# Performance work log

Hardware: AMD Instinct MI355X
Metric: run time of the kernel (lower is better)

Reference implementation:

```python
import jax, jax.numpy as jnp
import numpy as np

N_NODES = 100000
N_EDGES = 3200000
IN_DIM = 128


def setup_inputs() -> dict:
    key = jax.random.key(0)
    ks = jax.random.split(key, 6)
    x = jax.random.normal(ks[0], (N_NODES, IN_DIM), dtype=jnp.float32)
    edge_index = jax.random.randint(ks[1], (2, N_EDGES), 0, N_NODES, dtype=jnp.int64)
    # Glorot-ish init for weights, zero bias (PyG GCNConv default has bias)
    W1 = jax.random.normal(ks[2], (IN_DIM, 32), dtype=jnp.float32) / np.sqrt(IN_DIM)
    b1 = jnp.zeros((32,), dtype=jnp.float32)
    W2 = jax.random.normal(ks[3], (32, 16), dtype=jnp.float32) / np.sqrt(32.0)
    b2 = jnp.zeros((16,), dtype=jnp.float32)
    Wf = jax.random.normal(ks[4], (16, 1), dtype=jnp.float32) / np.sqrt(16.0)
    bf = jnp.zeros((1,), dtype=jnp.float32)
    return {"x": x, "edge_index": edge_index, "W1": W1, "b1": b1,
            "W2": W2, "b2": b2, "Wf": Wf, "bf": bf}


def reference(x, edge_index, W1, b1, W2, b2, Wf, bf):
    N = x.shape[0]
    # PyG GCNConv: add self-loops, symmetric normalization D^-1/2 (A+I) D^-1/2
    loop = jnp.arange(N, dtype=edge_index.dtype)
    src = jnp.concatenate([edge_index[0], loop])  # message sources (x_j)
    dst = jnp.concatenate([edge_index[1], loop])  # aggregation targets
    deg = jax.ops.segment_sum(jnp.ones_like(dst, dtype=x.dtype), dst, num_segments=N)
    dinv = jax.lax.rsqrt(jnp.maximum(deg, 1.0))  # deg >= 1 due to self-loops
    norm = dinv[src] * dinv[dst]                  # per-edge coefficient

    def gcn_conv(h, W, b):
        h = h @ W                                 # linear transform first (small dim)
        msg = h[src] * norm[:, None]              # gather + scale
        return jax.ops.segment_sum(msg, dst, num_segments=N) + b  # scatter-add

    h = jax.nn.relu(gcn_conv(x, W1, b1))
    h = jax.nn.relu(gcn_conv(h, W2, b2))
    return (h @ Wf + bf).squeeze(-1)              # [N]
```

## Files before the change

kernel.cpp:

```cpp
#include <hip/hip_runtime.h>


#define TPB 256
#define NBUCK 512
#define BCAP 8192
#define CHUNK 4096

__device__ __forceinline__ unsigned f2bf(float f) {
    unsigned u = __float_as_uint(f);
    return (u + 0x7FFFu + ((u >> 16) & 1u)) >> 16;
}
__device__ __forceinline__ float bflo(unsigned u) { return __uint_as_float(u << 16); }
__device__ __forceinline__ float bfhi(unsigned u) { return __uint_as_float(u & 0xFFFF0000u); }

__device__ __forceinline__ int excl_scan_512(int v, int* wsum, int tid) {
    int lane = tid & 63, wv = tid >> 6;
    int x = v;
#pragma unroll
    for (int d = 1; d < 64; d <<= 1) {
        int y = __shfl_up(x, d, 64);
        if (lane >= d) x += y;
    }
    if (lane == 63) wsum[wv] = x;
    __syncthreads();
    if (tid < 64) {
        int s = (lane < 8) ? wsum[lane] : 0;
#pragma unroll
        for (int d = 1; d < 8; d <<= 1) {
            int y = __shfl_up(s, d, 64);
            if (lane >= d) s += y;
        }
        if (lane < 8) wsum[lane] = s;
    }
    __syncthreads();
    int base = (wv > 0) ? wsum[wv - 1] : 0;
    return base + x - v;
}

__global__ __launch_bounds__(512) void binA2_kernel(
        const int* __restrict__ src, const int* __restrict__ dst,
        int* __restrict__ bcur, unsigned* __restrict__ staging, int E, int NPB) {
    __shared__ unsigned packed[CHUNK];
    __shared__ unsigned short buckb[CHUNK];
    __shared__ int hist[NBUCK];
    __shared__ int lstart[NBUCK];
    __shared__ int lcur[NBUCK];
    __shared__ int gbase[NBUCK];
    __shared__ int wsum[8];
    int tid = threadIdx.x;
    int start = blockIdx.x * CHUNK;
    int sz = min(CHUNK, E - start);

    unsigned dreg[8], sreg[8];
    hist[tid] = 0;
#pragma unroll
    for (int c = 0; c < 8; ++c) {
        int i = tid + c * 512;
        if (i < sz) {
            dreg[c] = (unsigned)dst[start + i];
            sreg[c] = (unsigned)src[start + i];
        } else {
            dreg[c] = 0xFFFFFFFFu;
        }
    }
    __syncthreads();
#pragma unroll
    for (int c = 0; c < 8; ++c)
        if (dreg[c] != 0xFFFFFFFFu) atomicAdd(&hist[dreg[c] / (unsigned)NPB], 1);
    __syncthreads();
    int v = hist[tid];
    int excl = excl_scan_512(v, wsum, tid);
    lstart[tid] = excl;
    lcur[tid] = 0;
    gbase[tid] = atomicAdd(&bcur[tid], v);
    __syncthreads();
#pragma unroll
    for (int c = 0; c < 8; ++c) {
        if (dreg[c] == 0xFFFFFFFFu) continue;
        unsigned d = dreg[c];
        unsigned b = d / (unsigned)NPB;
        unsigned loc = d - b * (unsigned)NPB;
        int pos = atomicAdd(&lcur[b], 1);
        int si = lstart[b] + pos;
        packed[si] = (loc << 20) | sreg[c];
        buckb[si] = (unsigned short)b;
    }
    __syncthreads();
    for (int i = tid; i < sz; i += 512) {
        unsigned b = buckb[i];
        int dsti = gbase[b] + (i - lstart[b]);
        if (dsti < BCAP)
            staging[(size_t)b * BCAP + dsti] = packed[i];
    }
}

__global__ __launch_bounds__(512) void bbase_kernel(
        const int* __restrict__ bcur, int* __restrict__ bbase) {
    __shared__ int wsum[8];
    int tid = threadIdx.x;
    int v = min(bcur[tid], BCAP);
    bbase[tid] = excl_scan_512(v, wsum, tid);
}

__global__ __launch_bounds__(512) void buildB_kernel(
        const int* __restrict__ bcur, const int* __restrict__ bbase,
        const unsigned* __restrict__ staging,
        int* __restrict__ offs, int* __restrict__ counts,
        float* __restrict__ dinv, int* __restrict__ csr_src,
        int N, int NPB) {
    __shared__ int hist[512];
    __shared__ int cur[512];
    __shared__ int wsum[8];
    int b = blockIdx.x;
    int tid = threadIdx.x;
    int sz = min(bcur[b], BCAP);
    int base = bbase[b];
    int n0 = b * NPB;
    int nn = min(NPB, N - n0);
    const unsigned* se = staging + (size_t)b * BCAP;

    unsigned preg[16];
    hist[tid] = 0;
#pragma unroll
    for (int c = 0; c < 16; ++c) {
        int i = tid + c * 512;
        preg[c] = (i < sz) ? se[i] : 0xFFFFFFFFu;
    }
    __syncthreads();
#pragma unroll
    for (int c = 0; c < 16; ++c)
        if (preg[c] != 0xFFFFFFFFu) atomicAdd(&hist[preg[c] >> 20], 1);
    __syncthreads();
    int h = hist[tid];
    int excl = excl_scan_512(h, wsum, tid);
    cur[tid] = excl;
    if (tid < nn) {
        int node = n0 + tid;
        offs[node] = base + excl;
        counts[node] = h;
        dinv[node] = rsqrtf((float)(h + 1));
    }
    __syncthreads();
#pragma unroll
    for (int c = 0; c < 16; ++c) {
        unsigned p = preg[c];
        if (p == 0xFFFFFFFFu) continue;
        int pos = atomicAdd(&cur[p >> 20], 1);
        csr_src[base + pos] = (int)(p & 0xFFFFFu);
    }
}

__global__ __launch_bounds__(256) void gemm1_kernel(
        const float* __restrict__ x, const float* __restrict__ W1,
        const float* __restrict__ dinv, unsigned* __restrict__ xwd, int N) {
    __shared__ float ws_[128 * 32];
    for (int i = threadIdx.x; i < 128 * 32; i += 256) ws_[i] = W1[i];
    __syncthreads();
    int t = threadIdx.x;
    int jq = (t & 3) * 8;
    int n0 = blockIdx.x * 128 + (t >> 2) * 2;
    if (n0 >= N) return;
    int nc0 = min(n0 + 0, N - 1);
    int nc1 = min(n0 + 1, N - 1);
    const float4* xr0 = (const float4*)(x + (size_t)nc0 * 128);
    const float4* xr1 = (const float4*)(x + (size_t)nc1 * 128);
    float acc[2][8];
#pragma unroll
    for (int n = 0; n < 2; ++n)
#pragma unroll
        for (int j = 0; j < 8; ++j) acc[n][j] = 0.0f;
#pragma unroll 2
    for (int k4 = 0; k4 < 32; ++k4) {
        const float* wb = ws_ + (k4 * 4) * 32 + jq;
        float4 a0 = *(const float4*)(wb);
        float4 a1 = *(const float4*)(wb + 4);
        float4 b0 = *(const float4*)(wb + 32);
        float4 b1v = *(const float4*)(wb + 36);
        float4 c0 = *(const float4*)(wb + 64);
        float4 c1 = *(const float4*)(wb + 68);
        float4 d0 = *(const float4*)(wb + 96);
        float4 d1 = *(const float4*)(wb + 100);
        float4 xv0 = xr0[k4];
        float4 xv1 = xr1[k4];
#pragma unroll
        for (int n = 0; n < 2; ++n) {
            float4 xv = (n == 0) ? xv0 : xv1;
            acc[n][0] += xv.x * a0.x + xv.y * b0.x + xv.z * c0.x + xv.w * d0.x;
            acc[n][1] += xv.x * a0.y + xv.y * b0.y + xv.z * c0.y + xv.w * d0.y;
            acc[n][2] += xv.x * a0.z + xv.y * b0.z + xv.z * c0.z + xv.w * d0.z;
            acc[n][3] += xv.x * a0.w + xv.y * b0.w + xv.z * c0.w + xv.w * d0.w;
            acc[n][4] += xv.x * a1.x + xv.y * b1v.x + xv.z * c1.x + xv.w * d1.x;
            acc[n][5] += xv.x * a1.y + xv.y * b1v.y + xv.z * c1.y + xv.w * d1.y;
            acc[n][6] += xv.x * a1.z + xv.y * b1v.z + xv.z * c1.z + xv.w * d1.z;
            acc[n][7] += xv.x * a1.w + xv.y * b1v.w + xv.z * c1.w + xv.w * d1.w;
        }
    }
#pragma unroll
    for (int n = 0; n < 2; ++n) {
        int node = n0 + n;
        if (node >= N) break;
        float d = dinv[node];
        unsigned pk0 = f2bf(acc[n][0] * d) | (f2bf(acc[n][1] * d) << 16);
        unsigned pk1 = f2bf(acc[n][2] * d) | (f2bf(acc[n][3] * d) << 16);
        unsigned pk2 = f2bf(acc[n][4] * d) | (f2bf(acc[n][5] * d) << 16);
        unsigned pk3 = f2bf(acc[n][6] * d) | (f2bf(acc[n][7] * d) << 16);
        ((uint4*)(xwd + (size_t)node * 16))[t & 3] = make_uint4(pk0, pk1, pk2, pk3);
    }
}

__global__ __launch_bounds__(256) void aggF_kernel(
        const int* __restrict__ offs, const int* __restrict__ counts,
        const int* __restrict__ csr_src, const float* __restrict__ dinv,
        const unsigned* __restrict__ xwd, const float* __restrict__ b1,
        const float* __restrict__ W2, unsigned* __restrict__ h2wd, int N) {
    __shared__ float ws2[32 * 16];
    for (int i = threadIdx.x; i < 512; i += 256) ws2[i] = W2[i];
    __syncthreads();
    int t = threadIdx.x;
    int q = t & 3;
    int node = blockIdx.x * 64 + (t >> 2);
    if (node >= N) return;
    int off = offs[node];
    int deg = counts[node];
    float acc[8];
    {
        uint4 v = ((const uint4*)(xwd + (size_t)node * 16))[q];
        acc[0] = bflo(v.x); acc[1] = bfhi(v.x);
        acc[2] = bflo(v.y); acc[3] = bfhi(v.y);
        acc[4] = bflo(v.z); acc[5] = bfhi(v.z);
        acc[6] = bflo(v.w); acc[7] = bfhi(v.w);
    }
    int deg8 = deg & ~7;
    int idx[8];
    if (deg8 > 0) {
#pragma unroll
        for (int c = 0; c < 8; ++c) idx[c] = csr_src[off + c];
    }
    int i = 0;
    while (i < deg8) {
        uint4 v0 = ((const uint4*)(xwd + (size_t)idx[0] * 16))[q];
        uint4 v1 = ((const uint4*)(xwd + (size_t)idx[1] * 16))[q];
        uint4 v2 = ((const uint4*)(xwd + (size_t)idx[2] * 16))[q];
        uint4 v3 = ((const uint4*)(xwd + (size_t)idx[3] * 16))[q];
        uint4 v4 = ((const uint4*)(xwd + (size_t)idx[4] * 16))[q];
        uint4 v5 = ((const uint4*)(xwd + (size_t)idx[5] * 16))[q];
        uint4 v6 = ((const uint4*)(xwd + (size_t)idx[6] * 16))[q];
        uint4 v7 = ((const uint4*)(xwd + (size_t)idx[7] * 16))[q];
        i += 8;
        if (i < deg8) {
#pragma unroll
            for (int c = 0; c < 8; ++c) idx[c] = csr_src[off + i + c];
        }
        acc[0] += ((bflo(v0.x) + bflo(v1.x)) + (bflo(v2.x) + bflo(v3.x)))
                + ((bflo(v4.x) + bflo(v5.x)) + (bflo(v6.x) + bflo(v7.x)));
        acc[1] += ((bfhi(v0.x) + bfhi(v1.x)) + (bfhi(v2.x) + bfhi(v3.x)))
                + ((bfhi(v4.x) + bfhi(v5.x)) + (bfhi(v6.x) + bfhi(v7.x)));
        acc[2] += ((bflo(v0.y) + bflo(v1.y)) + (bflo(v2.y) + bflo(v3.y)))
                + ((bflo(v4.y) + bflo(v5.y)) + (bflo(v6.y) + bflo(v7.y)));
        acc[3] += ((bfhi(v0.y) + bfhi(v1.y)) + (bfhi(v2.y) + bfhi(v3.y)))
                + ((bfhi(v4.y) + bfhi(v5.y)) + (bfhi(v6.y) + bfhi(v7.y)));
        acc[4] += ((bflo(v0.z) + bflo(v1.z)) + (bflo(v2.z) + bflo(v3.z)))
                + ((bflo(v4.z) + bflo(v5.z)) + (bflo(v6.z) + bflo(v7.z)));
        acc[5] += ((bfhi(v0.z) + bfhi(v1.z)) + (bfhi(v2.z) + bfhi(v3.z)))
                + ((bfhi(v4.z) + bfhi(v5.z)) + (bfhi(v6.z) + bfhi(v7.z)));
        acc[6] += ((bflo(v0.w) + bflo(v1.w)) + (bflo(v2.w) + bflo(v3.w)))
                + ((bflo(v4.w) + bflo(v5.w)) + (bflo(v6.w) + bflo(v7.w)));
        acc[7] += ((bfhi(v0.w) + bfhi(v1.w)) + (bfhi(v2.w) + bfhi(v3.w)))
                + ((bfhi(v4.w) + bfhi(v5.w)) + (bfhi(v6.w) + bfhi(v7.w)));
    }
    for (; i < deg; ++i) {
        int s = csr_src[off + i];
        uint4 v = ((const uint4*)(xwd + (size_t)s * 16))[q];
        acc[0] += bflo(v.x); acc[1] += bfhi(v.x);
        acc[2] += bflo(v.y); acc[3] += bfhi(v.y);
        acc[4] += bflo(v.z); acc[5] += bfhi(v.z);
        acc[6] += bflo(v.w); acc[7] += bfhi(v.w);
    }
    float dv = dinv[node];
    float part[16];
#pragma unroll
    for (int j = 0; j < 16; ++j) part[j] = 0.0f;
    const float* bq = b1 + q * 8;
#pragma unroll
    for (int k = 0; k < 8; ++k) {
        float h = fmaxf(acc[k] * dv + bq[k], 0.0f);
        const float* wr = ws2 + (q * 8 + k) * 16;
        float4 w0 = *(const float4*)(wr);
        float4 w1 = *(const float4*)(wr + 4);
        float4 w2 = *(const float4*)(wr + 8);
        float4 w3 = *(const float4*)(wr + 12);
        part[0]  += h * w0.x; part[1]  += h * w0.y; part[2]  += h * w0.z; part[3]  += h * w0.w;
        part[4]  += h * w1.x; part[5]  += h * w1.y; part[6]  += h * w1.z; part[7]  += h * w1.w;
        part[8]  += h * w2.x; part[9]  += h * w2.y; part[10] += h * w2.z; part[11] += h * w2.w;
        part[12] += h * w3.x; part[13] += h * w3.y; part[14] += h * w3.z; part[15] += h * w3.w;
    }
    float p8[8];
#pragma unroll
    for (int j = 0; j < 8; ++j) {
        float send = (q & 1) ? part[j] : part[j + 8];
        float keep = (q & 1) ? part[j + 8] : part[j];
        p8[j] = keep + __shfl_xor(send, 1, 64);
    }
    float p4[4];
#pragma unroll
    for (int j = 0; j < 4; ++j) {
        float send = (q & 2) ? p8[j] : p8[j + 4];
        float keep = (q & 2) ? p8[j + 4] : p8[j];
        p4[j] = keep + __shfl_xor(send, 2, 64);
    }
    unsigned pk0 = f2bf(p4[0] * dv) | (f2bf(p4[1] * dv) << 16);
    unsigned pk1 = f2bf(p4[2] * dv) | (f2bf(p4[3] * dv) << 16);
    int slot = ((q & 1) << 1) | ((q >> 1) & 1);
    ((uint2*)(h2wd + (size_t)node * 8))[slot] = make_uint2(pk0, pk1);
}

__global__ __launch_bounds__(256) void aggS16f_kernel(
        const int* __restrict__ offs, const int* __restrict__ counts,
        const int* __restrict__ csr_src, const float* __restrict__ dinv,
        const unsigned* __restrict__ h2wd,
        const float* __restrict__ b2, const float* __restrict__ Wf,
        const float* __restrict__ bf, float* __restrict__ out, int N) {
    __shared__ float bs_[16];
    __shared__ float wf_[16];
    __shared__ float bfv;
    int t = threadIdx.x;
    if (t < 16) { bs_[t] = b2[t]; wf_[t] = Wf[t]; }
    if (t == 0) bfv = bf[0];
    __syncthreads();
    int q = t & 1;
    int node = blockIdx.x * 128 + (t >> 1);
    if (node >= N) return;
    int off = offs[node];
    int deg = counts[node];
    float acc[8];
    {
        uint4 v = ((const uint4*)(h2wd + (size_t)node * 8))[q];
        acc[0] = bflo(v.x); acc[1] = bfhi(v.x);
        acc[2] = bflo(v.y); acc[3] = bfhi(v.y);
        acc[4] = bflo(v.z); acc[5] = bfhi(v.z);
        acc[6] = bflo(v.w); acc[7] = bfhi(v.w);
    }
    int deg8 = deg & ~7;
    int idx[8];
    if (deg8 > 0) {
#pragma unroll
        for (int c = 0; c < 8; ++c) idx[c] = csr_src[off + c];
    }
    int i = 0;
    while (i < deg8) {
        uint4 v0 = ((const uint4*)(h2wd + (size_t)idx[0] * 8))[q];
        uint4 v1 = ((const uint4*)(h2wd + (size_t)idx[1] * 8))[q];
        uint4 v2 = ((const uint4*)(h2wd + (size_t)idx[2] * 8))[q];
        uint4 v3 = ((const uint4*)(h2wd + (size_t)idx[3] * 8))[q];
        uint4 v4 = ((const uint4*)(h2wd + (size_t)idx[4] * 8))[q];
        uint4 v5 = ((const uint4*)(h2wd + (size_t)idx[5] * 8))[q];
        uint4 v6 = ((const uint4*)(h2wd + (size_t)idx[6] * 8))[q];
        uint4 v7 = ((const uint4*)(h2wd + (size_t)idx[7] * 8))[q];
        i += 8;
        if (i < deg8) {
#pragma unroll
            for (int c = 0; c < 8; ++c) idx[c] = csr_src[off + i + c];
        }
        acc[0] += ((bflo(v0.x) + bflo(v1.x)) + (bflo(v2.x) + bflo(v3.x)))
                + ((bflo(v4.x) + bflo(v5.x)) + (bflo(v6.x) + bflo(v7.x)));
        acc[1] += ((bfhi(v0.x) + bfhi(v1.x)) + (bfhi(v2.x) + bfhi(v3.x)))
                + ((bfhi(v4.x) + bfhi(v5.x)) + (bfhi(v6.x) + bfhi(v7.x)));
        acc[2] += ((bflo(v0.y) + bflo(v1.y)) + (bflo(v2.y) + bflo(v3.y)))
                + ((bflo(v4.y) + bflo(v5.y)) + (bflo(v6.y) + bflo(v7.y)));
        acc[3] += ((bfhi(v0.y) + bfhi(v1.y)) + (bfhi(v2.y) + bfhi(v3.y)))
                + ((bfhi(v4.y) + bfhi(v5.y)) + (bfhi(v6.y) + bfhi(v7.y)));
        acc[4] += ((bflo(v0.z) + bflo(v1.z)) + (bflo(v2.z) + bflo(v3.z)))
                + ((bflo(v4.z) + bflo(v5.z)) + (bflo(v6.z) + bflo(v7.z)));
        acc[5] += ((bfhi(v0.z) + bfhi(v1.z)) + (bfhi(v2.z) + bfhi(v3.z)))
                + ((bfhi(v4.z) + bfhi(v5.z)) + (bfhi(v6.z) + bfhi(v7.z)));
        acc[6] += ((bflo(v0.w) + bflo(v1.w)) + (bflo(v2.w) + bflo(v3.w)))
                + ((bflo(v4.w) + bflo(v5.w)) + (bflo(v6.w) + bflo(v7.w)));
        acc[7] += ((bfhi(v0.w) + bfhi(v1.w)) + (bfhi(v2.w) + bfhi(v3.w)))
                + ((bfhi(v4.w) + bfhi(v5.w)) + (bfhi(v6.w) + bfhi(v7.w)));
    }
    for (; i < deg; ++i) {
        int s = csr_src[off + i];
        uint4 v = ((const uint4*)(h2wd + (size_t)s * 8))[q];
        acc[0] += bflo(v.x); acc[1] += bfhi(v.x);
        acc[2] += bflo(v.y); acc[3] += bfhi(v.y);
        acc[4] += bflo(v.z); acc[5] += bfhi(v.z);
        acc[6] += bflo(v.w); acc[7] += bfhi(v.w);
    }
    float dv = dinv[node];
    const float* bq = bs_ + q * 8;
    const float* wq = wf_ + q * 8;
    float part = 0.f;
#pragma unroll
    for (int k = 0; k < 8; ++k)
        part += fmaxf(acc[k] * dv + bq[k], 0.f) * wq[k];
    part += __shfl_xor(part, 1, 64);
    if (q == 0) out[node] = part + bfv;
}

extern "C" void kernel_launch(void* const* d_in, const int* in_sizes, int n_in,
                              void* d_out, int out_size, void* d_ws, size_t ws_size,
                              hipStream_t stream) {
    const float* x  = (const float*)d_in[0];
    const int*   ei = (const int*)d_in[1];
    const float* W1 = (const float*)d_in[2];
    const float* b1 = (const float*)d_in[3];
    const float* W2 = (const float*)d_in[4];
    const float* b2 = (const float*)d_in[5];
    const float* Wf = (const float*)d_in[6];
    const float* bf = (const float*)d_in[7];

    int N = in_sizes[0] / 128;
    int E = in_sizes[1] / 2;
    const int* src = ei;
    const int* dst = ei + E;
    int NPB = (N + NBUCK - 1) / NBUCK;

    size_t Np = ((size_t)N + 3) & ~(size_t)3;
    size_t Ep = ((size_t)E + 3) & ~(size_t)3;
    int* wsI      = (int*)d_ws;
    int* counts   = wsI;
    int* offs     = counts + Np;
    int* bcur     = offs + Np;
    int* bbase    = bcur + NBUCK;
    int* csr_src  = bbase + NBUCK;
    float* dinv   = (float*)(csr_src + Ep);
    unsigned* xwd = (unsigned*)(dinv + Np);
    unsigned* staging = xwd + 16 * Np;
    unsigned* h2wd = staging;
    float* out    = (float*)d_out;

    int nbC  = (E + CHUNK - 1) / CHUNK;
    int nbG1 = (N + 127) / 128;
    int nbA32 = (N + 63) / 64;
    int nbA16 = (N + 127) / 128;

    hipMemsetAsync(bcur, 0, NBUCK * sizeof(int), stream);
    binA2_kernel<<<nbC, 512, 0, stream>>>(src, dst, bcur, staging, E, NPB);
    bbase_kernel<<<1, 512, 0, stream>>>(bcur, bbase);
    buildB_kernel<<<NBUCK, 512, 0, stream>>>(bcur, bbase, staging, offs, counts,
                                             dinv, csr_src, N, NPB);
    gemm1_kernel<<<nbG1, 256, 0, stream>>>(x, W1, dinv, xwd, N);
    aggF_kernel<<<nbA32, 256, 0, stream>>>(offs, counts, csr_src, dinv, xwd,
                                           b1, W2, h2wd, N);
    aggS16f_kernel<<<nbA16, 256, 0, stream>>>(offs, counts, csr_src, dinv, h2wd,
                                              b2, Wf, bf, out, N);
}
```

Baseline: 244.7 us.

## Fuse CSR build stages into one cooperative kernel with grid sync

Merges the binning, bucket-base scan and per-bucket CSR build kernels into a single cooperative kernel launched with one block per bucket. Blocks grid-stride over the edge chunks, then use a grid-wide sync before each block redundantly scans the bucket counts and builds its own bucket. This removes two kernel launches and the inter-kernel gaps, at the cost of a grid barrier and fewer blocks (512) for the binning phase, which had about 782 chunks.

```diff
diff --git a/kernel.cpp b/kernel.cpp
--- a/kernel.cpp
+++ b/kernel.cpp
@@ -1,4 +1,7 @@
 #include <hip/hip_runtime.h>
+#include <hip/hip_cooperative_groups.h>
+
+namespace cg = cooperative_groups;
 
 
 #define TPB 256
@@ -37,9 +40,13 @@
     return base + x - v;
 }
 
-__global__ __launch_bounds__(512) void binA2_kernel(
+__global__ __launch_bounds__(512, 4) void build_kernel(
         const int* __restrict__ src, const int* __restrict__ dst,
-        int* __restrict__ bcur, unsigned* __restrict__ staging, int E, int NPB) {
+        int* __restrict__ bcur, unsigned* __restrict__ staging,
+        int* __restrict__ offs, int* __restrict__ counts,
+        float* __restrict__ dinv, int* __restrict__ csr_src,
+        int E, int N, int NPB, int nchunks) {
+    cg::grid_group grid = cg::this_grid();
     __shared__ unsigned packed[CHUNK];
     __shared__ unsigned short buckb[CHUNK];
     __shared__ int hist[NBUCK];
@@ -48,95 +55,88 @@
     __shared__ int gbase[NBUCK];
     __shared__ int wsum[8];
     int tid = threadIdx.x;
-    int start = blockIdx.x * CHUNK;
-    int sz = min(CHUNK, E - start);
-
-    unsigned dreg[8], sreg[8];
+
+    for (int chunk = blockIdx.x; chunk < nchunks; chunk += gridDim.x) {
+        int start = chunk * CHUNK;
+        int sz = min(CHUNK, E - start);
+        __syncthreads();
+        unsigned dreg[8], sreg[8];
+        hist[tid] = 0;
+#pragma unroll
+        for (int c = 0; c < 8; ++c) {
+            int i = tid + c * 512;
+            if (i < sz) {
+                dreg[c] = (unsigned)dst[start + i];
+                sreg[c] = (unsigned)src[start + i];
+            } else {
+                dreg[c] = 0xFFFFFFFFu;
+            }
+        }
+        __syncthreads();
+#pragma unroll
+        for (int c = 0; c < 8; ++c)
+            if (dreg[c] != 0xFFFFFFFFu)
+                atomicAdd(&hist[dreg[c] / (unsigned)NPB], 1);
+        __syncthreads();
+        int v = hist[tid];
+        int excl = excl_scan_512(v, wsum, tid);
+        lstart[tid] = excl;
+        lcur[tid] = 0;
+        gbase[tid] = atomicAdd(&bcur[tid], v);
+        __syncthreads();
+#pragma unroll
+        for (int c = 0; c < 8; ++c) {
+            if (dreg[c] == 0xFFFFFFFFu) continue;
+            unsigned d = dreg[c];
+            unsigned b = d / (unsigned)NPB;
+            unsigned loc = d - b * (unsigned)NPB;
+            int pos = atomicAdd(&lcur[b], 1);
+            int si = lstart[b] + pos;
+            packed[si] = (loc << 20) | sreg[c];
+            buckb[si] = (unsigned short)b;
+        }
+        __syncthreads();
+        for (int i = tid; i < sz; i += 512) {
+            unsigned b = buckb[i];
+            int dsti = gbase[b] + (i - lstart[b]);
+            if (dsti < BCAP)
+                staging[(size_t)b * BCAP + dsti] = packed[i];
+        }
+    }
+
+    __threadfence();
+    grid.sync();
+    __threadfence();
+
+    int b = blockIdx.x;
+    int bcv = bcur[tid];
+    int myv = min(bcv, BCAP);
+    int excl = excl_scan_512(myv, wsum, tid);
+    gbase[tid] = excl;
     hist[tid] = 0;
-#pragma unroll
-    for (int c = 0; c < 8; ++c) {
-        int i = tid + c * 512;
-        if (i < sz) {
-            dreg[c] = (unsigned)dst[start + i];
-            sreg[c] = (unsigned)src[start + i];
-        } else {
-            dreg[c] = 0xFFFFFFFFu;
-        }
-    }
-    __syncthreads();
-#pragma unroll
-    for (int c = 0; c < 8; ++c)
-        if (dreg[c] != 0xFFFFFFFFu) atomicAdd(&hist[dreg[c] / (unsigned)NPB], 1);
-    __syncthreads();
-    int v = hist[tid];
-    int excl = excl_scan_512(v, wsum, tid);
-    lstart[tid] = excl;
-    lcur[tid] = 0;
-    gbase[tid] = atomicAdd(&bcur[tid], v);
-    __syncthreads();
-#pragma unroll
-    for (int c = 0; c < 8; ++c) {
-        if (dreg[c] == 0xFFFFFFFFu) continue;
-        unsigned d = dreg[c];
-        unsigned b = d / (unsigned)NPB;
-        unsigned loc = d - b * (unsigned)NPB;
-        int pos = atomicAdd(&lcur[b], 1);
-        int si = lstart[b] + pos;
-        packed[si] = (loc << 20) | sreg[c];
-        buckb[si] = (unsigned short)b;
-    }
-    __syncthreads();
-    for (int i = tid; i < sz; i += 512) {
-        unsigned b = buckb[i];
-        int dsti = gbase[b] + (i - lstart[b]);
-        if (dsti < BCAP)
-            staging[(size_t)b * BCAP + dsti] = packed[i];
-    }
-}
-
-__global__ __launch_bounds__(512) void bbase_kernel(
-        const int* __restrict__ bcur, int* __restrict__ bbase) {
-    __shared__ int wsum[8];
-    int tid = threadIdx.x;
-    int v = min(bcur[tid], BCAP);
-    bbase[tid] = excl_scan_512(v, wsum, tid);
-}
-
-__global__ __launch_bounds__(512) void buildB_kernel(
-        const int* __restrict__ bcur, const int* __restrict__ bbase,
-        const unsigned* __restrict__ staging,
-        int* __restrict__ offs, int* __restrict__ counts,
-        float* __restrict__ dinv, int* __restrict__ csr_src,
-        int N, int NPB) {
-    __shared__ int hist[512];
-    __shared__ int cur[512];
-    __shared__ int wsum[8];
-    int b = blockIdx.x;
-    int tid = threadIdx.x;
+    __syncthreads();
+    int base = gbase[b];
     int sz = min(bcur[b], BCAP);
-    int base = bbase[b];
     int n0 = b * NPB;
     int nn = min(NPB, N - n0);
     const unsigned* se = staging + (size_t)b * BCAP;
 
     unsigned preg[16];
-    hist[tid] = 0;
 #pragma unroll
     for (int c = 0; c < 16; ++c) {
         int i = tid + c * 512;
         preg[c] = (i < sz) ? se[i] : 0xFFFFFFFFu;
     }
-    __syncthreads();
 #pragma unroll
     for (int c = 0; c < 16; ++c)
         if (preg[c] != 0xFFFFFFFFu) atomicAdd(&hist[preg[c] >> 20], 1);
     __syncthreads();
     int h = hist[tid];
-    int excl = excl_scan_512(h, wsum, tid);
-    cur[tid] = excl;
+    int excl2 = excl_scan_512(h, wsum, tid);
+    lstart[tid] = excl2;
     if (tid < nn) {
         int node = n0 + tid;
-        offs[node] = base + excl;
+        offs[node] = base + excl2;
         counts[node] = h;
         dinv[node] = rsqrtf((float)(h + 1));
     }
@@ -145,7 +145,7 @@
     for (int c = 0; c < 16; ++c) {
         unsigned p = preg[c];
         if (p == 0xFFFFFFFFu) continue;
-        int pos = atomicAdd(&cur[p >> 20], 1);
+        int pos = atomicAdd(&lstart[p >> 20], 1);
         csr_src[base + pos] = (int)(p & 0xFFFFFu);
     }
 }
@@ -421,24 +421,24 @@
     int* counts   = wsI;
     int* offs     = counts + Np;
     int* bcur     = offs + Np;
-    int* bbase    = bcur + NBUCK;
-    int* csr_src  = bbase + NBUCK;
+    int* csr_src  = bcur + NBUCK;
     float* dinv   = (float*)(csr_src + Ep);
     unsigned* xwd = (unsigned*)(dinv + Np);
     unsigned* staging = xwd + 16 * Np;
     unsigned* h2wd = staging;
     float* out    = (float*)d_out;
 
-    int nbC  = (E + CHUNK - 1) / CHUNK;
+    int nchunks = (E + CHUNK - 1) / CHUNK;
     int nbG1 = (N + 127) / 128;
     int nbA32 = (N + 63) / 64;
     int nbA16 = (N + 127) / 128;
 
     hipMemsetAsync(bcur, 0, NBUCK * sizeof(int), stream);
-    binA2_kernel<<<nbC, 512, 0, stream>>>(src, dst, bcur, staging, E, NPB);
-    bbase_kernel<<<1, 512, 0, stream>>>(bcur, bbase);
-    buildB_kernel<<<NBUCK, 512, 0, stream>>>(bcur, bbase, staging, offs, counts,
-                                             dinv, csr_src, N, NPB);
+    void* cargs[] = {(void*)&src, (void*)&dst, (void*)&bcur, (void*)&staging,
+                     (void*)&offs, (void*)&counts, (void*)&dinv, (void*)&csr_src,
+                     (void*)&E, (void*)&N, (void*)&NPB, (void*)&nchunks};
+    hipLaunchCooperativeKernel((void*)build_kernel, dim3(NBUCK), dim3(512),
+                               cargs, 0, stream);
     gemm1_kernel<<<nbG1, 256, 0, stream>>>(x, W1, dinv, xwd, N);
     aggF_kernel<<<nbA32, 256, 0, stream>>>(offs, counts, csr_src, dinv, xwd,
                                            b1, W2, h2wd, N);
```

After: 492.9 us. 2.01x slower.

## Split node edge lists across two thread groups and fuse bucket scan into buildB

Applied to the files above, without the earlier changes.

Each destination node's neighbor list in both aggregation kernels is now split between two thread groups, and the partial sums are combined with a lane shuffle. This doubles the threads working on each node and halves the serial gather chain per thread. Separately, the single-block bucket-base scan kernel is removed; every buildB block recomputes the 512-entry scan itself, saving one launch at the cost of redundant scan work. The partner threads duplicate the epilogue math, and twice as many blocks are launched.

```diff
diff --git a/kernel.cpp b/kernel.cpp
--- a/kernel.cpp
+++ b/kernel.cpp
@@ -94,27 +94,21 @@
     }
 }
 
-__global__ __launch_bounds__(512) void bbase_kernel(
-        const int* __restrict__ bcur, int* __restrict__ bbase) {
-    __shared__ int wsum[8];
-    int tid = threadIdx.x;
-    int v = min(bcur[tid], BCAP);
-    bbase[tid] = excl_scan_512(v, wsum, tid);
-}
-
 __global__ __launch_bounds__(512) void buildB_kernel(
-        const int* __restrict__ bcur, const int* __restrict__ bbase,
-        const unsigned* __restrict__ staging,
+        const int* __restrict__ bcur, const unsigned* __restrict__ staging,
         int* __restrict__ offs, int* __restrict__ counts,
         float* __restrict__ dinv, int* __restrict__ csr_src,
         int N, int NPB) {
     __shared__ int hist[512];
     __shared__ int cur[512];
     __shared__ int wsum[8];
+    __shared__ int base_sh;
     int b = blockIdx.x;
     int tid = threadIdx.x;
+    int myv = min(bcur[tid], BCAP);
+    int bexcl = excl_scan_512(myv, wsum, tid);
+    if (tid == b) base_sh = bexcl;
     int sz = min(bcur[b], BCAP);
-    int base = bbase[b];
     int n0 = b * NPB;
     int nn = min(NPB, N - n0);
     const unsigned* se = staging + (size_t)b * BCAP;
@@ -127,6 +121,7 @@
         preg[c] = (i < sz) ? se[i] : 0xFFFFFFFFu;
     }
     __syncthreads();
+    int base = base_sh;
 #pragma unroll
     for (int c = 0; c < 16; ++c)
         if (preg[c] != 0xFFFFFFFFu) atomicAdd(&hist[preg[c] >> 20], 1);
@@ -218,23 +213,30 @@
     __syncthreads();
     int t = threadIdx.x;
     int q = t & 3;
-    int node = blockIdx.x * 64 + (t >> 2);
+    int h = (t >> 2) & 1;
+    int node = blockIdx.x * 32 + (t >> 3);
     if (node >= N) return;
     int off = offs[node];
     int deg = counts[node];
+    int d0 = (deg + 1) >> 1;
+    int mydeg = h ? (deg - d0) : d0;
+    int myoff = off + (h ? d0 : 0);
     float acc[8];
-    {
+    if (h == 0) {
         uint4 v = ((const uint4*)(xwd + (size_t)node * 16))[q];
         acc[0] = bflo(v.x); acc[1] = bfhi(v.x);
         acc[2] = bflo(v.y); acc[3] = bfhi(v.y);
         acc[4] = bflo(v.z); acc[5] = bfhi(v.z);
         acc[6] = bflo(v.w); acc[7] = bfhi(v.w);
-    }
-    int deg8 = deg & ~7;
+    } else {
+#pragma unroll
+        for (int j = 0; j < 8; ++j) acc[j] = 0.0f;
+    }
+    int deg8 = mydeg & ~7;
     int idx[8];
     if (deg8 > 0) {
 #pragma unroll
-        for (int c = 0; c < 8; ++c) idx[c] = csr_src[off + c];
+        for (int c = 0; c < 8; ++c) idx[c] = csr_src[myoff + c];
     }
     int i = 0;
     while (i < deg8) {
@@ -249,7 +251,7 @@
         i += 8;
         if (i < deg8) {
 #pragma unroll
-            for (int c = 0; c < 8; ++c) idx[c] = csr_src[off + i + c];
+            for (int c = 0; c < 8; ++c) idx[c] = csr_src[myoff + i + c];
         }
         acc[0] += ((bflo(v0.x) + bflo(v1.x)) + (bflo(v2.x) + bflo(v3.x)))
                 + ((bflo(v4.x) + bflo(v5.x)) + (bflo(v6.x) + bflo(v7.x)));
@@ -268,14 +270,16 @@
         acc[7] += ((bfhi(v0.w) + bfhi(v1.w)) + (bfhi(v2.w) + bfhi(v3.w)))
                 + ((bfhi(v4.w) + bfhi(v5.w)) + (bfhi(v6.w) + bfhi(v7.w)));
     }
-    for (; i < deg; ++i) {
-        int s = csr_src[off + i];
+    for (; i < mydeg; ++i) {
+        int s = csr_src[myoff + i];
         uint4 v = ((const uint4*)(xwd + (size_t)s * 16))[q];
         acc[0] += bflo(v.x); acc[1] += bfhi(v.x);
         acc[2] += bflo(v.y); acc[3] += bfhi(v.y);
         acc[4] += bflo(v.z); acc[5] += bfhi(v.z);
         acc[6] += bflo(v.w); acc[7] += bfhi(v.w);
     }
+#pragma unroll
+    for (int j = 0; j < 8; ++j) acc[j] += __shfl_xor(acc[j], 4, 64);
     float dv = dinv[node];
     float part[16];
 #pragma unroll
@@ -283,16 +287,16 @@
     const float* bq = b1 + q * 8;
 #pragma unroll
     for (int k = 0; k < 8; ++k) {
-        float h = fmaxf(acc[k] * dv + bq[k], 0.0f);
+        float hh = fmaxf(acc[k] * dv + bq[k], 0.0f);
         const float* wr = ws2 + (q * 8 + k) * 16;
         float4 w0 = *(const float4*)(wr);
         float4 w1 = *(const float4*)(wr + 4);
         float4 w2 = *(const float4*)(wr + 8);
         float4 w3 = *(const float4*)(wr + 12);
-        part[0]  += h * w0.x; part[1]  += h * w0.y; part[2]  += h * w0.z; part[3]  += h * w0.w;
-        part[4]  += h * w1.x; part[5]  += h * w1.y; part[6]  += h * w1.z; part[7]  += h * w1.w;
-        part[8]  += h * w2.x; part[9]  += h * w2.y; part[10] += h * w2.z; part[11] += h * w2.w;
-        part[12] += h * w3.x; part[13] += h * w3.y; part[14] += h * w3.z; part[15] += h * w3.w;
+        part[0]  += hh * w0.x; part[1]  += hh * w0.y; part[2]  += hh * w0.z; part[3]  += hh * w0.w;
+        part[4]  += hh * w1.x; part[5]  += hh * w1.y; part[6]  += hh * w1.z; part[7]  += hh * w1.w;
+        part[8]  += hh * w2.x; part[9]  += hh * w2.y; part[10] += hh * w2.z; part[11] += hh * w2.w;
+        part[12] += hh * w3.x; part[13] += hh * w3.y; part[14] += hh * w3.z; part[15] += hh * w3.w;
     }
     float p8[8];
 #pragma unroll
@@ -311,7 +315,8 @@
     unsigned pk0 = f2bf(p4[0] * dv) | (f2bf(p4[1] * dv) << 16);
     unsigned pk1 = f2bf(p4[2] * dv) | (f2bf(p4[3] * dv) << 16);
     int slot = ((q & 1) << 1) | ((q >> 1) & 1);
-    ((uint2*)(h2wd + (size_t)node * 8))[slot] = make_uint2(pk0, pk1);
+    if (h == 0)
+        ((uint2*)(h2wd + (size_t)node * 8))[slot] = make_uint2(pk0, pk1);
 }
 
 __global__ __launch_bounds__(256) void aggS16f_kernel(
@@ -328,23 +333,30 @@
     if (t == 0) bfv = bf[0];
     __syncthreads();
     int q = t & 1;
-    int node = blockIdx.x * 128 + (t >> 1);
+    int h = (t >> 1) & 1;
+    int node = blockIdx.x * 64 + (t >> 2);
     if (node >= N) return;
     int off = offs[node];
     int deg = counts[node];
+    int d0 = (deg + 1) >> 1;
+    int mydeg = h ? (deg - d0) : d0;
+    int myoff = off + (h ? d0 : 0);
     float acc[8];
-    {
+    if (h == 0) {
         uint4 v = ((const uint4*)(h2wd + (size_t)node * 8))[q];
         acc[0] = bflo(v.x); acc[1] = bfhi(v.x);
         acc[2] = bflo(v.y); acc[3] = bfhi(v.y);
         acc[4] = bflo(v.z); acc[5] = bfhi(v.z);
         acc[6] = bflo(v.w); acc[7] = bfhi(v.w);
-    }
-    int deg8 = deg & ~7;
+    } else {
+#pragma unroll
+        for (int j = 0; j < 8; ++j) acc[j] = 0.0f;
+    }
+    int deg8 = mydeg & ~7;
     int idx[8];
     if (deg8 > 0) {
 #pragma unroll
-        for (int c = 0; c < 8; ++c) idx[c] = csr_src[off + c];
+        for (int c = 0; c < 8; ++c) idx[c] = csr_src[myoff + c];
     }
     int i = 0;
     while (i < deg8) {
@@ -359,7 +371,7 @@
         i += 8;
         if (i < deg8) {
 #pragma unroll
-            for (int c = 0; c < 8; ++c) idx[c] = csr_src[off + i + c];
+            for (int c = 0; c < 8; ++c) idx[c] = csr_src[myoff + i + c];
         }
         acc[0] += ((bflo(v0.x) + bflo(v1.x)) + (bflo(v2.x) + bflo(v3.x)))
                 + ((bflo(v4.x) + bflo(v5.x)) + (bflo(v6.x) + bflo(v7.x)));
@@ -378,14 +390,16 @@
         acc[7] += ((bfhi(v0.w) + bfhi(v1.w)) + (bfhi(v2.w) + bfhi(v3.w)))
                 + ((bfhi(v4.w) + bfhi(v5.w)) + (bfhi(v6.w) + bfhi(v7.w)));
     }
-    for (; i < deg; ++i) {
-        int s = csr_src[off + i];
+    for (; i < mydeg; ++i) {
+        int s = csr_src[myoff + i];
         uint4 v = ((const uint4*)(h2wd + (size_t)s * 8))[q];
         acc[0] += bflo(v.x); acc[1] += bfhi(v.x);
         acc[2] += bflo(v.y); acc[3] += bfhi(v.y);
         acc[4] += bflo(v.z); acc[5] += bfhi(v.z);
         acc[6] += bflo(v.w); acc[7] += bfhi(v.w);
     }
+#pragma unroll
+    for (int j = 0; j < 8; ++j) acc[j] += __shfl_xor(acc[j], 2, 64);
     float dv = dinv[node];
     const float* bq = bs_ + q * 8;
     const float* wq = wf_ + q * 8;
@@ -394,7 +408,7 @@
     for (int k = 0; k < 8; ++k)
         part += fmaxf(acc[k] * dv + bq[k], 0.f) * wq[k];
     part += __shfl_xor(part, 1, 64);
-    if (q == 0) out[node] = part + bfv;
+    if ((t & 3) == 0) out[node] = part + bfv;
 }
 
 extern "C" void kernel_launch(void* const* d_in, const int* in_sizes, int n_in,
@@ -421,8 +435,7 @@
     int* counts   = wsI;
     int* offs     = counts + Np;
     int* bcur     = offs + Np;
-    int* bbase    = bcur + NBUCK;
-    int* csr_src  = bbase + NBUCK;
+    int* csr_src  = bcur + NBUCK;
     float* dinv   = (float*)(csr_src + Ep);
     unsigned* xwd = (unsigned*)(dinv + Np);
     unsigned* staging = xwd + 16 * Np;
@@ -431,13 +444,12 @@
 
     int nbC  = (E + CHUNK - 1) / CHUNK;
     int nbG1 = (N + 127) / 128;
-    int nbA32 = (N + 63) / 64;
-    int nbA16 = (N + 127) / 128;
+    int nbA32 = (N + 31) / 32;
+    int nbA16 = (N + 63) / 64;
 
     hipMemsetAsync(bcur, 0, NBUCK * sizeof(int), stream);
     binA2_kernel<<<nbC, 512, 0, stream>>>(src, dst, bcur, staging, E, NPB);
-    bbase_kernel<<<1, 512, 0, stream>>>(bcur, bbase);
-    buildB_kernel<<<NBUCK, 512, 0, stream>>>(bcur, bbase, staging, offs, counts,
+    buildB_kernel<<<NBUCK, 512, 0, stream>>>(bcur, staging, offs, counts,
                                              dinv, csr_src, N, NPB);
     gemm1_kernel<<<nbG1, 256, 0, stream>>>(x, W1, dinv, xwd, N);
     aggF_kernel<<<nbA32, 256, 0, stream>>>(offs, counts, csr_src, dinv, xwd,
```

Result: no change. 245.5 us (+0.3%).
